# Kernel tuning notes

Measured on AMD Instinct MI355X. Metric: run time of the kernel, lower is better.

## Reference

```python
import jax, jax.numpy as jnp
import numpy as np

D_MODEL = 1024
N_HEADS = 16
N_KV_HEADS = 4
HEAD_DIM = 64


def setup_inputs() -> dict:
    key = jax.random.key(0)
    ks = jax.random.split(key, 5)
    B, T, P = 2, 512, 8
    scale = 1.0 / np.sqrt(D_MODEL)
    return {
        "hidden_states": jax.random.normal(ks[0], (B, T, P, D_MODEL), dtype=jnp.float32),
        # weights stored [in, out] so y = x @ W (same math as nn.Linear with W^T)
        "Wq": jax.random.normal(ks[1], (D_MODEL, N_HEADS * HEAD_DIM), dtype=jnp.float32) * scale,
        "Wk": jax.random.normal(ks[2], (D_MODEL, N_KV_HEADS * HEAD_DIM), dtype=jnp.float32) * scale,
        "Wv": jax.random.normal(ks[3], (D_MODEL, N_KV_HEADS * HEAD_DIM), dtype=jnp.float32) * scale,
        "Wo": jax.random.normal(ks[4], (N_HEADS * HEAD_DIM, D_MODEL), dtype=jnp.float32) * scale,
    }


def _rope_tables(T, d):
    half = d // 2
    inv_freq = 1.0 / (10000.0 ** (jnp.arange(half, dtype=jnp.float32) / half))
    pos = jnp.arange(T, dtype=jnp.float32)
    angles = pos[:, None] * inv_freq[None, :]  # (T, half)
    return jnp.cos(angles), jnp.sin(angles)


def _apply_rope(x, cos, sin):
    # x: (B, P, T, H, d); cos/sin: (T, d/2)
    half = x.shape[-1] // 2
    x1, x2 = x[..., :half], x[..., half:]
    c = cos[None, None, :, None, :]
    s = sin[None, None, :, None, :]
    return jnp.concatenate([x1 * c - x2 * s, x1 * s + x2 * c], axis=-1)


def reference(hidden_states, Wq, Wk, Wv, Wo):
    B, T, P, _ = hidden_states.shape
    x = jnp.transpose(hidden_states, (0, 2, 1, 3))  # (B, P, T, C)
    q = (x @ Wq).reshape(B, P, T, N_HEADS, HEAD_DIM)
    k = (x @ Wk).reshape(B, P, T, N_KV_HEADS, HEAD_DIM)
    v = (x @ Wv).reshape(B, P, T, N_KV_HEADS, HEAD_DIM)

    rep = N_HEADS // N_KV_HEADS
    k = jnp.repeat(k, rep, axis=3)  # (B,P,T,H,d) interleaved like torch repeat/view
    v = jnp.repeat(v, rep, axis=3)

    cos, sin = _rope_tables(T, HEAD_DIM)
    q = _apply_rope(q, cos, sin)
    k = _apply_rope(k, cos, sin)

    # (B,P,H,T,d)
    q = jnp.transpose(q, (0, 1, 3, 2, 4))
    k = jnp.transpose(k, (0, 1, 3, 2, 4))
    v = jnp.transpose(v, (0, 1, 3, 2, 4))

    attn = jnp.einsum("bphqd,bphkd->bphqk", q, k) / jnp.sqrt(
        jnp.asarray(HEAD_DIM, q.dtype))
    attn = jax.nn.softmax(attn, axis=-1)
    out = jnp.einsum("bphqk,bphkd->bphqd", attn, v)
    out = jnp.transpose(out, (0, 1, 3, 2, 4)).reshape(B, P, T, N_HEADS * HEAD_DIM)
    out = jnp.transpose(out, (0, 2, 1, 3))  # (B, T, P, H*d)
    return out @ Wo
```

## Files before the change

kernel.cpp:

```cpp
#include <hip/hip_runtime.h>
#include <stdint.h>


typedef __attribute__((ext_vector_type(8))) short bf16x8;
typedef __attribute__((ext_vector_type(4))) float f32x4;
typedef __attribute__((ext_vector_type(16))) float f32x16;
typedef __attribute__((ext_vector_type(4))) unsigned short us4;
typedef __attribute__((ext_vector_type(8))) unsigned short us8;

static __device__ __forceinline__ unsigned short f2bf(float f) {
  unsigned u = __float_as_uint(f);
  u += 0x7fffu + ((u >> 16) & 1u);
  return (unsigned short)(u >> 16);
}

static __device__ __forceinline__ void ld_lds16(const void* g, void* l) {
  __builtin_amdgcn_global_load_lds(
      (const __attribute__((address_space(1))) void*)g,
      (__attribute__((address_space(3))) void*)l, 16, 0, 0);
}

static __device__ __forceinline__ f32x4 mfma16(bf16x8 a, bf16x8 b, f32x4 c) {
  return __builtin_amdgcn_mfma_f32_16x16x32_bf16(a, b, c, 0, 0, 0);
}
static __device__ __forceinline__ f32x16 mfma32(bf16x8 a, bf16x8 b, f32x16 c) {
  return __builtin_amdgcn_mfma_f32_32x32x16_bf16(a, b, c, 0, 0, 0);
}

__global__ __launch_bounds__(256) void conv_all(
    const float* __restrict__ hs, const float* __restrict__ Wq,
    const float* __restrict__ Wk, const float* __restrict__ Wv,
    const float* __restrict__ Wo, unsigned short* __restrict__ xb,
    unsigned short* __restrict__ wqkv, unsigned short* __restrict__ wot) {
  __shared__ float tile[64][65];
  int bid = blockIdx.x, tid = threadIdx.x;
  if (bid < 8192) {
    int gid = bid * 256 + tid;
    size_t e = (size_t)gid * 4;
    int r = (int)(e >> 10);
    int d = (int)(e & 1023);
    int b = r >> 12, p = (r >> 9) & 7, t = r & 511;
    const float4* src = (const float4*)(hs + ((((size_t)b * 512 + t) * 8 + p) << 10) + d);
    float4 v = *src;
    us4 o;
    o.x = f2bf(v.x); o.y = f2bf(v.y); o.z = f2bf(v.z); o.w = f2bf(v.w);
    *(us4*)(xb + e) = o;
    return;
  }
  int tb = bid - 8192;
  const float* W; unsigned short* Wt; int N, tc0, tn0;
  if (tb < 256)      { W = Wq; Wt = wqkv;                       N = 1024; tc0 = (tb >> 4) * 64;          tn0 = (tb & 15) * 64; }
  else if (tb < 320) { W = Wk; Wt = wqkv + (size_t)1024 * 1024; N = 256;  tc0 = ((tb - 256) >> 2) * 64;  tn0 = ((tb - 256) & 3) * 64; }
  else if (tb < 384) { W = Wv; Wt = wqkv + (size_t)1280 * 1024; N = 256;  tc0 = ((tb - 320) >> 2) * 64;  tn0 = ((tb - 320) & 3) * 64; }
  else               { W = Wo; Wt = wot;                        N = 1024; tc0 = ((tb - 384) >> 4) * 64;  tn0 = ((tb - 384) & 15) * 64; }
  int tr = tid >> 4, tc = tid & 15;
#pragma unroll
  for (int i = 0; i < 4; ++i) {
    int c = tr + i * 16;
    float4 v = *(const float4*)(W + (size_t)(tc0 + c) * N + tn0 + tc * 4);
    tile[c][tc * 4 + 0] = v.x; tile[c][tc * 4 + 1] = v.y;
    tile[c][tc * 4 + 2] = v.z; tile[c][tc * 4 + 3] = v.w;
  }
  __syncthreads();
#pragma unroll
  for (int i = 0; i < 4; ++i) {
    int n = tr + i * 16;
    us4 o;
    o.x = f2bf(tile[tc * 4 + 0][n]); o.y = f2bf(tile[tc * 4 + 1][n]);
    o.z = f2bf(tile[tc * 4 + 2][n]); o.w = f2bf(tile[tc * 4 + 3][n]);
    *(us4*)(Wt + (size_t)(tn0 + n) * 1024 + tc0 + tc * 4) = o;
  }
}

__global__ __launch_bounds__(512, 2) void gemm_qkv(
    const unsigned short* __restrict__ A, const unsigned short* __restrict__ Bt,
    unsigned short* __restrict__ qb, unsigned short* __restrict__ kb,
    unsigned short* __restrict__ vtb) {
  constexpr int K = 1024;
  constexpr int KT = K / 64;
  __shared__ __align__(16) unsigned short Sm[2][2][256 * 64];
  unsigned short* Cs = &Sm[0][0][0];

  int tid = threadIdx.x;
  int lane = tid & 63, wid = tid >> 6;
  int quad = lane >> 4, lo = lane & 15;
  int wg = (blockIdx.x & 7) * 24 + (blockIdx.x >> 3);
  int tn = wg % 6, tm = wg / 6;
  int wr = wid >> 2, wc = wid & 3;
  int srow = lane >> 3, schunk = lane & 7;
  int cg = schunk ^ srow;

  const unsigned short* pa = A + ((size_t)(tm * 256) + wid * 8 + srow) * K + cg * 8;
  const unsigned short* pb = Bt + ((size_t)(tn * 256) + wid * 8 + srow) * K + cg * 8;

  f32x4 z = {0.f, 0.f, 0.f, 0.f};
  f32x4 acc[8][4];
#pragma unroll
  for (int i = 0; i < 8; ++i)
#pragma unroll
    for (int j = 0; j < 4; ++j) acc[i][j] = z;

  auto stage = [&](int t, int p) {
#pragma unroll
    for (int i = 0; i < 4; ++i) {
      ld_lds16(pa + (size_t)i * 64 * K + t * 64,
               (char*)&Sm[p][0][0] + (wid * 8 + i * 64) * 128);
      ld_lds16(pb + (size_t)i * 64 * K + t * 64,
               (char*)&Sm[p][1][0] + (wid * 8 + i * 64) * 128);
    }
  };

  stage(0, 0);
  stage(1, 1);
  asm volatile("s_waitcnt vmcnt(8)" ::: "memory");
  asm volatile("s_barrier" ::: "memory");

  bf16x8 af[4][2], bb0[2][2], bb1[2][2];

  for (int t = 0; t < KT; ++t) {
    int p = t & 1;
    const unsigned short* As = &Sm[p][0][0];
    const unsigned short* Bs = &Sm[p][1][0];

#pragma unroll
    for (int mi = 0; mi < 4; ++mi)
#pragma unroll
      for (int kx = 0; kx < 2; ++kx) {
        int row = wr * 128 + mi * 16 + lo;
        int cgx = (quad + kx * 4) ^ (row & 7);
        af[mi][kx] = *(const bf16x8*)(As + (size_t)row * 64 + cgx * 8);
      }
#pragma unroll
    for (int ni = 0; ni < 2; ++ni)
#pragma unroll
      for (int kx = 0; kx < 2; ++kx) {
        int row = wc * 64 + ni * 16 + lo;
        int cgx = (quad + kx * 4) ^ (row & 7);
        bb0[ni][kx] = *(const bf16x8*)(Bs + (size_t)row * 64 + cgx * 8);
      }
    asm volatile("s_barrier" ::: "memory");
    __builtin_amdgcn_s_setprio(1);
#pragma unroll
    for (int kx = 0; kx < 2; ++kx)
#pragma unroll
      for (int mi = 0; mi < 4; ++mi)
#pragma unroll
        for (int ni = 0; ni < 2; ++ni)
          acc[mi][ni] = mfma16(af[mi][kx], bb0[ni][kx], acc[mi][ni]);
    __builtin_amdgcn_s_setprio(0);
    asm volatile("s_barrier" ::: "memory");

#pragma unroll
    for (int ni = 0; ni < 2; ++ni)
#pragma unroll
      for (int kx = 0; kx < 2; ++kx) {
        int row = wc * 64 + (ni + 2) * 16 + lo;
        int cgx = (quad + kx * 4) ^ (row & 7);
        bb1[ni][kx] = *(const bf16x8*)(Bs + (size_t)row * 64 + cgx * 8);
      }
    asm volatile("s_barrier" ::: "memory");
    __builtin_amdgcn_s_setprio(1);
#pragma unroll
    for (int kx = 0; kx < 2; ++kx)
#pragma unroll
      for (int mi = 0; mi < 4; ++mi)
#pragma unroll
        for (int ni = 0; ni < 2; ++ni)
          acc[mi][ni + 2] = mfma16(af[mi][kx], bb1[ni][kx], acc[mi][ni + 2]);
    __builtin_amdgcn_s_setprio(0);
    asm volatile("s_barrier" ::: "memory");

#pragma unroll
    for (int mi = 0; mi < 4; ++mi)
#pragma unroll
      for (int kx = 0; kx < 2; ++kx) {
        int row = wr * 128 + 64 + mi * 16 + lo;
        int cgx = (quad + kx * 4) ^ (row & 7);
        af[mi][kx] = *(const bf16x8*)(As + (size_t)row * 64 + cgx * 8);
      }
    asm volatile("s_barrier" ::: "memory");
    __builtin_amdgcn_s_setprio(1);
#pragma unroll
    for (int kx = 0; kx < 2; ++kx)
#pragma unroll
      for (int mi = 0; mi < 4; ++mi)
#pragma unroll
        for (int ni = 0; ni < 2; ++ni)
          acc[mi + 4][ni + 2] = mfma16(af[mi][kx], bb1[ni][kx], acc[mi + 4][ni + 2]);
    __builtin_amdgcn_s_setprio(0);
    asm volatile("s_barrier" ::: "memory");

    bool pf = (t + 2 < KT);
    if (pf) stage(t + 2, p);
    __builtin_amdgcn_s_setprio(1);
#pragma unroll
    for (int kx = 0; kx < 2; ++kx)
#pragma unroll
      for (int mi = 0; mi < 4; ++mi)
#pragma unroll
        for (int ni = 0; ni < 2; ++ni)
          acc[mi + 4][ni] = mfma16(af[mi][kx], bb0[ni][kx], acc[mi + 4][ni]);
    __builtin_amdgcn_s_setprio(0);
    if (pf) asm volatile("s_waitcnt vmcnt(8)" ::: "memory");
    else    asm volatile("s_waitcnt vmcnt(0)" ::: "memory");
    asm volatile("s_barrier" ::: "memory");
  }

  if (tn < 5) {
    float qscale = (tn < 4) ? 0.125f : 1.0f;
#pragma unroll
    for (int mi = 0; mi < 8; ++mi)
#pragma unroll
      for (int r = 0; r < 4; ++r) {
        int row = wr * 128 + mi * 16 + quad * 4 + r;
        int tpos = (tm * 256 + row) & 511;
#pragma unroll
        for (int ni = 0; ni < 2; ++ni) {
          float invf = exp2f((float)(ni * 16 + lo) * -0.41524101186092029f);
          float ang = (float)tpos * invf;
          float s, c;
          __sincosf(ang, &s, &c);
          float x1 = acc[mi][ni][r], x2 = acc[mi][ni + 2][r];
          acc[mi][ni][r]     = (x1 * c - x2 * s) * qscale;
          acc[mi][ni + 2][r] = (x1 * s + x2 * c) * qscale;
        }
      }
#pragma unroll
    for (int mi = 0; mi < 8; ++mi)
#pragma unroll
      for (int ni = 0; ni < 4; ++ni)
#pragma unroll
        for (int r = 0; r < 4; ++r) {
          int row = wr * 128 + mi * 16 + quad * 4 + r;
          int col = wc * 64 + ni * 16 + lo;
          int cs = col ^ (((row >> 2) & 3) << 3);
          Cs[row * 256 + cs] = f2bf(acc[mi][ni][r]);
        }
    __syncthreads();
    int tc = tid & 31, ro = tid >> 5;
#pragma unroll
    for (int it = 0; it < 16; ++it) {
      int row = ro + 16 * it;
      int cs = (tc * 8) ^ (((row >> 2) & 3) << 3);
      us8 v = *(const us8*)(Cs + row * 256 + cs);
      size_t grow = (size_t)(tm * 256 + row);
      if (tn < 4) *(us8*)(qb + grow * 1024 + tn * 256 + tc * 8) = v;
      else        *(us8*)(kb + grow * 256 + tc * 8) = v;
    }
  } else {
#pragma unroll
    for (int mi = 0; mi < 8; ++mi)
#pragma unroll
      for (int ni = 0; ni < 4; ++ni)
#pragma unroll
        for (int r = 0; r < 4; ++r) {
          int trow = wr * 128 + mi * 16 + quad * 4 + r;
          int col = wc * 64 + ni * 16 + lo;
          Cs[col * 256 + (trow ^ ((col & 7) << 3))] = f2bf(acc[mi][ni][r]);
        }
    __syncthreads();
    int t0 = (tid & 31) * 8, colIdx = tid >> 5;
    int bp = tm >> 1, tbase = (tm & 1) * 256;
#pragma unroll
    for (int it = 0; it < 16; ++it) {
      int col = colIdx + it * 16;
      us8 v = *(const us8*)(Cs + col * 256 + (t0 ^ ((col & 7) << 3)));
      int hh = col >> 6, dd = col & 63;
      *(us8*)(vtb + (((size_t)(bp * 4 + hh)) * 64 + dd) * 512 + tbase + t0) = v;
    }
  }
}

__global__ __launch_bounds__(512, 2) void gemm_o(
    const unsigned short* __restrict__ A, const unsigned short* __restrict__ Bt,
    float* __restrict__ out) {
  constexpr int K = 1024;
  constexpr int KT = K / 64;
  __shared__ __align__(16) unsigned short Sm[2][(128 + 256) * 64];

  int tid = threadIdx.x;
  int lane = tid & 63, wid = tid >> 6;
  int quad = lane >> 4, lo = lane & 15;
  int wg = (blockIdx.x & 7) * 32 + (blockIdx.x >> 3);
  int tn = wg & 3, tm = wg >> 2;
  int wr = wid >> 2, wc = wid & 3;
  int srow = lane >> 3, schunk = lane & 7;
  int cg = schunk ^ srow;

  const unsigned short* pa = A + ((size_t)(tm * 128) + wid * 8 + srow) * K + cg * 8;
  const unsigned short* pb = Bt + ((size_t)(tn * 256) + wid * 8 + srow) * K + cg * 8;

  f32x4 z = {0.f, 0.f, 0.f, 0.f};
  f32x4 acc[4][4];
#pragma unroll
  for (int i = 0; i < 4; ++i)
#pragma unroll
    for (int j = 0; j < 4; ++j) acc[i][j] = z;

  auto stage = [&](int t, int p) {
    unsigned short* As = &Sm[p][0];
    unsigned short* Bs = &Sm[p][128 * 64];
#pragma unroll
    for (int i = 0; i < 2; ++i)
      ld_lds16(pa + (size_t)i * 64 * K + t * 64,
               (char*)As + (wid * 8 + i * 64) * 128);
#pragma unroll
    for (int i = 0; i < 4; ++i)
      ld_lds16(pb + (size_t)i * 64 * K + t * 64,
               (char*)Bs + (wid * 8 + i * 64) * 128);
  };

  stage(0, 0);
  stage(1, 1);
  asm volatile("s_waitcnt vmcnt(6)" ::: "memory");
  asm volatile("s_barrier" ::: "memory");

  bf16x8 af[4][2], bb0[2][2], bb1[2][2];

  for (int t = 0; t < KT; ++t) {
    int p = t & 1;
    const unsigned short* As = &Sm[p][0];
    const unsigned short* Bs = &Sm[p][128 * 64];

#pragma unroll
    for (int mi = 0; mi < 4; ++mi)
#pragma unroll
      for (int kx = 0; kx < 2; ++kx) {
        int row = wr * 64 + mi * 16 + lo;
        int cgx = (quad + kx * 4) ^ (row & 7);
        af[mi][kx] = *(const bf16x8*)(As + (size_t)row * 64 + cgx * 8);
      }
#pragma unroll
    for (int ni = 0; ni < 2; ++ni)
#pragma unroll
      for (int kx = 0; kx < 2; ++kx) {
        int row = wc * 64 + ni * 16 + lo;
        int cgx = (quad + kx * 4) ^ (row & 7);
        bb0[ni][kx] = *(const bf16x8*)(Bs + (size_t)row * 64 + cgx * 8);
      }
    asm volatile("s_barrier" ::: "memory");
    __builtin_amdgcn_s_setprio(1);
#pragma unroll
    for (int kx = 0; kx < 2; ++kx)
#pragma unroll
      for (int mi = 0; mi < 4; ++mi)
#pragma unroll
        for (int ni = 0; ni < 2; ++ni)
          acc[mi][ni] = mfma16(af[mi][kx], bb0[ni][kx], acc[mi][ni]);
    __builtin_amdgcn_s_setprio(0);
    asm volatile("s_barrier" ::: "memory");

#pragma unroll
    for (int ni = 0; ni < 2; ++ni)
#pragma unroll
      for (int kx = 0; kx < 2; ++kx) {
        int row = wc * 64 + (ni + 2) * 16 + lo;
        int cgx = (quad + kx * 4) ^ (row & 7);
        bb1[ni][kx] = *(const bf16x8*)(Bs + (size_t)row * 64 + cgx * 8);
      }
    asm volatile("s_barrier" ::: "memory");
    __builtin_amdgcn_s_setprio(1);
#pragma unroll
    for (int kx = 0; kx < 2; ++kx)
#pragma unroll
      for (int mi = 0; mi < 4; ++mi)
#pragma unroll
        for (int ni = 0; ni < 2; ++ni)
          acc[mi][ni + 2] = mfma16(af[mi][kx], bb1[ni][kx], acc[mi][ni + 2]);
    __builtin_amdgcn_s_setprio(0);
    asm volatile("s_barrier" ::: "memory");

    bool pf = (t + 2 < KT);
    if (pf) {
      stage(t + 2, p);
      asm volatile("s_waitcnt vmcnt(6)" ::: "memory");
    } else {
      asm volatile("s_waitcnt vmcnt(0)" ::: "memory");
    }
    asm volatile("s_barrier" ::: "memory");
  }

#pragma unroll
  for (int mi = 0; mi < 4; ++mi) {
    for (int ni = 0; ni < 4; ++ni) {
      int col = tn * 256 + wc * 64 + ni * 16 + lo;
      for (int r = 0; r < 4; ++r) {
        int grow = tm * 128 + wr * 64 + mi * 16 + quad * 4 + r;
        int bp = grow >> 9, tt = grow & 511;
        int b = bp >> 3, pp = bp & 7;
        out[((((size_t)b * 512 + tt) * 8 + pp) << 10) + col] = acc[mi][ni][r];
      }
    }
  }
}

__global__ __launch_bounds__(512, 4) void attn(
    const unsigned short* __restrict__ qb, const unsigned short* __restrict__ kb,
    const unsigned short* __restrict__ vtb, unsigned short* __restrict__ ao) {
  __shared__ __align__(16) unsigned short Qs[256 * 64];
  __shared__ __align__(16) unsigned short Ks[2][64 * 64];
  __shared__ __align__(16) unsigned short Vs[2][64 * 64];

  int tid = threadIdx.x;
  int lane = tid & 63, wid = tid >> 6;
  int lo32 = lane & 31, hl = lane >> 5;
  int wg = (blockIdx.x & 7) * 64 + (blockIdx.x >> 3);
  int qt = wg & 1, bph = wg >> 1;
  int head = bph & 15, bp = bph >> 4;
  int kvh = head >> 2;
  int t0 = qt * 256;
  int srow = lane >> 3, schunk = lane & 7;

  const unsigned short* qg = qb + ((size_t)(bp * 512 + t0)) * 1024 + head * 64;
  const unsigned short* kg = kb + ((size_t)bp * 512) * 256 + kvh * 64;
  const unsigned short* vg = vtb + ((size_t)(bp * 4 + kvh)) * 64 * 512;

#pragma unroll
  for (int i = 0; i < 4; ++i) {
    int row = wid * 8 + i * 64 + srow;
    int cg = schunk ^ (row & 7);
    ld_lds16(qg + (size_t)row * 1024 + cg * 8, (char*)Qs + (wid * 8 + i * 64) * 128);
  }

  auto stageKV = [&](int kt, int p) {
    int row = wid * 8 + srow;
    int cg = schunk ^ (row & 7);
    ld_lds16(kg + (size_t)(kt * 64 + row) * 256 + cg * 8, (char*)&Ks[p][0] + (wid * 8) * 128);
    ld_lds16(vg + (size_t)row * 512 + kt * 64 + cg * 8, (char*)&Vs[p][0] + (wid * 8) * 128);
  };

  stageKV(0, 0);
  stageKV(1, 1);
  asm volatile("s_waitcnt vmcnt(2)" ::: "memory");
  asm volatile("s_barrier" ::: "memory");

  f32x16 z16 = {0.f};
  f32x16 o0 = z16, o1 = z16;
  float psum = 0.f;
  int qrow = wid * 32 + lo32;

  for (int kt = 0; kt < 8; ++kt) {
    int p = kt & 1;
    const unsigned short* Kp = &Ks[p][0];
    const unsigned short* Vp = &Vs[p][0];

    f32x16 st0 = z16, st1 = z16;
#pragma unroll
    for (int kkc = 0; kkc < 4; ++kkc) {
      int ch = 2 * kkc + hl;
      bf16x8 qf = *(const bf16x8*)(Qs + (size_t)qrow * 64 + ((ch ^ (qrow & 7)) * 8));
      bf16x8 kf0 = *(const bf16x8*)(Kp + (size_t)lo32 * 64 + ((ch ^ (lo32 & 7)) * 8));
      bf16x8 kf1 = *(const bf16x8*)(Kp + (size_t)(32 + lo32) * 64 + ((ch ^ (lo32 & 7)) * 8));
      st0 = mfma32(kf0, qf, st0);
      st1 = mfma32(kf1, qf, st1);
    }

#pragma unroll
    for (int t = 0; t < 2; ++t) {
      const f32x16& stv = t ? st1 : st0;
      unsigned pk[8], xpk[8];
#pragma unroll
      for (int pp = 0; pp < 8; ++pp) {
        float e0 = __expf(stv[2 * pp]);
        float e1 = __expf(stv[2 * pp + 1]);
        psum += e0 + e1;
        pk[pp] = ((__float_as_uint(e0) + 0x8000u) >> 16) |
                 ((__float_as_uint(e1) + 0x8000u) & 0xffff0000u);
      }
#pragma unroll
      for (int pp = 0; pp < 8; ++pp) xpk[pp] = (unsigned)__shfl_xor((int)pk[pp], 32);
#pragma unroll
      for (int cc = 0; cc < 2; ++cc) {
        int o = cc * 4;
        union { unsigned u[4]; bf16x8 v; } af;
        if (hl == 0) {
          af.u[0] = pk[o];      af.u[1] = pk[o + 1];
          af.u[2] = xpk[o];     af.u[3] = xpk[o + 1];
        } else {
          af.u[0] = xpk[o + 2]; af.u[1] = xpk[o + 3];
          af.u[2] = pk[o + 2];  af.u[3] = pk[o + 3];
        }
        int vch = 2 * (t * 2 + cc) + hl;
        bf16x8 v0 = *(const bf16x8*)(Vp + (size_t)lo32 * 64 + ((vch ^ (lo32 & 7)) * 8));
        bf16x8 v1 = *(const bf16x8*)(Vp + (size_t)(32 + lo32) * 64 + ((vch ^ (lo32 & 7)) * 8));
        o0 = mfma32(af.v, v0, o0);
        o1 = mfma32(af.v, v1, o1);
      }
    }

    if (kt == 7) break;
    asm volatile("s_barrier" ::: "memory");
    if (kt < 6) {
      stageKV(kt + 2, p);
      asm volatile("s_waitcnt vmcnt(2)" ::: "memory");
    } else {
      asm volatile("s_waitcnt vmcnt(0)" ::: "memory");
    }
    asm volatile("s_barrier" ::: "memory");
  }

  psum += __shfl_xor(psum, 32);
  float inv = 1.f / psum;
#pragma unroll
  for (int r = 0; r < 16; ++r) {
    int q_r = (r & 3) + 8 * (r >> 2) + 4 * hl;
    float sc = __shfl(inv, q_r);
    size_t grow = (size_t)(bp * 512 + t0 + wid * 32 + q_r);
    ao[grow * 1024 + head * 64 + lo32]      = f2bf(o0[r] * sc);
    ao[grow * 1024 + head * 64 + 32 + lo32] = f2bf(o1[r] * sc);
  }
}

extern "C" void kernel_launch(void* const* d_in, const int* in_sizes, int n_in,
                              void* d_out, int out_size, void* d_ws, size_t ws_size,
                              hipStream_t stream) {
  const float* hs = (const float*)d_in[0];
  const float* Wq = (const float*)d_in[1];
  const float* Wk = (const float*)d_in[2];
  const float* Wv = (const float*)d_in[3];
  const float* Wo = (const float*)d_in[4];
  float* out = (float*)d_out;

  unsigned short* xb   = (unsigned short*)d_ws;
  unsigned short* wqkv = xb + (size_t)8192 * 1024;
  unsigned short* wot  = wqkv + (size_t)1536 * 1024;
  unsigned short* qbuf = wot + (size_t)1024 * 1024;
  unsigned short* kbuf = qbuf + (size_t)8192 * 1024;
  unsigned short* vtb  = kbuf + (size_t)8192 * 256;
  unsigned short* ao   = xb;

  conv_all<<<8832, 256, 0, stream>>>(hs, Wq, Wk, Wv, Wo, xb, wqkv, wot);
  gemm_qkv<<<192, 512, 0, stream>>>(xb, wqkv, qbuf, kbuf, vtb);
  attn<<<512, 512, 0, stream>>>(qbuf, kbuf, vtb, ao);
  gemm_o<<<256, 512, 0, stream>>>(ao, wot, out);
}
```

Measured before the change: 181.9 us.

## Process full 512-query block per workgroup with Q fragments held in registers

The attention kernel now gives each workgroup all 512 queries of a (batch, position, head) instead of 256, halving the grid, so each K/V tile staged in LDS is reused across twice as many queries. Q is loaded straight from global memory into registers rather than staged through LDS, and each wave handles two 32-row query groups per K/V tile. This is meant to cut repeated K/V global loads and LDS traffic. In exchange, register pressure goes up (launch bounds drop to 2 blocks per SIMD setting) and there are half as many workgroups, which could leave some of the chip's CUs underused.

```diff
diff --git a/kernel.cpp b/kernel.cpp
--- a/kernel.cpp
+++ b/kernel.cpp
@@ -394,39 +394,40 @@
   }
 }
 
-__global__ __launch_bounds__(512, 4) void attn(
-    const unsigned short* __restrict__ qb, const unsigned short* __restrict__ kb,
+__global__ __launch_bounds__(512, 2) void attn(
+    const unsigned short* __restrict__ qbuf, const unsigned short* __restrict__ kb,
     const unsigned short* __restrict__ vtb, unsigned short* __restrict__ ao) {
-  __shared__ __align__(16) unsigned short Qs[256 * 64];
   __shared__ __align__(16) unsigned short Ks[2][64 * 64];
   __shared__ __align__(16) unsigned short Vs[2][64 * 64];
 
   int tid = threadIdx.x;
   int lane = tid & 63, wid = tid >> 6;
   int lo32 = lane & 31, hl = lane >> 5;
-  int wg = (blockIdx.x & 7) * 64 + (blockIdx.x >> 3);
-  int qt = wg & 1, bph = wg >> 1;
-  int head = bph & 15, bp = bph >> 4;
+  int wg = (blockIdx.x & 7) * 32 + (blockIdx.x >> 3);
+  int head = wg & 15, bp = wg >> 4;
   int kvh = head >> 2;
-  int t0 = qt * 256;
   int srow = lane >> 3, schunk = lane & 7;
 
-  const unsigned short* qg = qb + ((size_t)(bp * 512 + t0)) * 1024 + head * 64;
   const unsigned short* kg = kb + ((size_t)bp * 512) * 256 + kvh * 64;
   const unsigned short* vg = vtb + ((size_t)(bp * 4 + kvh)) * 64 * 512;
 
-#pragma unroll
-  for (int i = 0; i < 4; ++i) {
-    int row = wid * 8 + i * 64 + srow;
-    int cg = schunk ^ (row & 7);
-    ld_lds16(qg + (size_t)row * 1024 + cg * 8, (char*)Qs + (wid * 8 + i * 64) * 128);
+  const unsigned short* qgA =
+      qbuf + ((size_t)(bp * 512 + wid * 64 + lo32)) * 1024 + head * 64;
+  bf16x8 qA[4], qB[4];
+#pragma unroll
+  for (int kkc = 0; kkc < 4; ++kkc) {
+    int ch = 2 * kkc + hl;
+    qA[kkc] = *(const bf16x8*)(qgA + ch * 8);
+    qB[kkc] = *(const bf16x8*)(qgA + (size_t)32 * 1024 + ch * 8);
   }
 
   auto stageKV = [&](int kt, int p) {
     int row = wid * 8 + srow;
     int cg = schunk ^ (row & 7);
-    ld_lds16(kg + (size_t)(kt * 64 + row) * 256 + cg * 8, (char*)&Ks[p][0] + (wid * 8) * 128);
-    ld_lds16(vg + (size_t)row * 512 + kt * 64 + cg * 8, (char*)&Vs[p][0] + (wid * 8) * 128);
+    ld_lds16(kg + (size_t)(kt * 64 + row) * 256 + cg * 8,
+             (char*)&Ks[p][0] + (wid * 8) * 128);
+    ld_lds16(vg + (size_t)row * 512 + kt * 64 + cg * 8,
+             (char*)&Vs[p][0] + (wid * 8) * 128);
   };
 
   stageKV(0, 0);
@@ -435,56 +436,71 @@
   asm volatile("s_barrier" ::: "memory");
 
   f32x16 z16 = {0.f};
-  f32x16 o0 = z16, o1 = z16;
-  float psum = 0.f;
-  int qrow = wid * 32 + lo32;
+  f32x16 oA0 = z16, oA1 = z16, oB0 = z16, oB1 = z16;
+  float psumA = 0.f, psumB = 0.f;
 
   for (int kt = 0; kt < 8; ++kt) {
     int p = kt & 1;
     const unsigned short* Kp = &Ks[p][0];
     const unsigned short* Vp = &Vs[p][0];
 
-    f32x16 st0 = z16, st1 = z16;
+    f32x16 sA0 = z16, sA1 = z16, sB0 = z16, sB1 = z16;
 #pragma unroll
     for (int kkc = 0; kkc < 4; ++kkc) {
       int ch = 2 * kkc + hl;
-      bf16x8 qf = *(const bf16x8*)(Qs + (size_t)qrow * 64 + ((ch ^ (qrow & 7)) * 8));
       bf16x8 kf0 = *(const bf16x8*)(Kp + (size_t)lo32 * 64 + ((ch ^ (lo32 & 7)) * 8));
       bf16x8 kf1 = *(const bf16x8*)(Kp + (size_t)(32 + lo32) * 64 + ((ch ^ (lo32 & 7)) * 8));
-      st0 = mfma32(kf0, qf, st0);
-      st1 = mfma32(kf1, qf, st1);
+      sA0 = mfma32(kf0, qA[kkc], sA0);
+      sA1 = mfma32(kf1, qA[kkc], sA1);
+      sB0 = mfma32(kf0, qB[kkc], sB0);
+      sB1 = mfma32(kf1, qB[kkc], sB1);
     }
 
 #pragma unroll
     for (int t = 0; t < 2; ++t) {
-      const f32x16& stv = t ? st1 : st0;
-      unsigned pk[8], xpk[8];
+      const f32x16& svA = t ? sA1 : sA0;
+      const f32x16& svB = t ? sB1 : sB0;
+      unsigned pkA[8], xpA[8], pkB[8], xpB[8];
 #pragma unroll
       for (int pp = 0; pp < 8; ++pp) {
-        float e0 = __expf(stv[2 * pp]);
-        float e1 = __expf(stv[2 * pp + 1]);
-        psum += e0 + e1;
-        pk[pp] = ((__float_as_uint(e0) + 0x8000u) >> 16) |
-                 ((__float_as_uint(e1) + 0x8000u) & 0xffff0000u);
-      }
-#pragma unroll
-      for (int pp = 0; pp < 8; ++pp) xpk[pp] = (unsigned)__shfl_xor((int)pk[pp], 32);
+        float a0 = __expf(svA[2 * pp]);
+        float a1 = __expf(svA[2 * pp + 1]);
+        psumA += a0 + a1;
+        pkA[pp] = ((__float_as_uint(a0) + 0x8000u) >> 16) |
+                  ((__float_as_uint(a1) + 0x8000u) & 0xffff0000u);
+        float b0 = __expf(svB[2 * pp]);
+        float b1 = __expf(svB[2 * pp + 1]);
+        psumB += b0 + b1;
+        pkB[pp] = ((__float_as_uint(b0) + 0x8000u) >> 16) |
+                  ((__float_as_uint(b1) + 0x8000u) & 0xffff0000u);
+      }
+#pragma unroll
+      for (int pp = 0; pp < 8; ++pp) {
+        xpA[pp] = (unsigned)__shfl_xor((int)pkA[pp], 32);
+        xpB[pp] = (unsigned)__shfl_xor((int)pkB[pp], 32);
+      }
 #pragma unroll
       for (int cc = 0; cc < 2; ++cc) {
         int o = cc * 4;
-        union { unsigned u[4]; bf16x8 v; } af;
+        union { unsigned u[4]; bf16x8 v; } fA, fB;
         if (hl == 0) {
-          af.u[0] = pk[o];      af.u[1] = pk[o + 1];
-          af.u[2] = xpk[o];     af.u[3] = xpk[o + 1];
+          fA.u[0] = pkA[o];     fA.u[1] = pkA[o + 1];
+          fA.u[2] = xpA[o];     fA.u[3] = xpA[o + 1];
+          fB.u[0] = pkB[o];     fB.u[1] = pkB[o + 1];
+          fB.u[2] = xpB[o];     fB.u[3] = xpB[o + 1];
         } else {
-          af.u[0] = xpk[o + 2]; af.u[1] = xpk[o + 3];
-          af.u[2] = pk[o + 2];  af.u[3] = pk[o + 3];
+          fA.u[0] = xpA[o + 2]; fA.u[1] = xpA[o + 3];
+          fA.u[2] = pkA[o + 2]; fA.u[3] = pkA[o + 3];
+          fB.u[0] = xpB[o + 2]; fB.u[1] = xpB[o + 3];
+          fB.u[2] = pkB[o + 2]; fB.u[3] = pkB[o + 3];
         }
         int vch = 2 * (t * 2 + cc) + hl;
         bf16x8 v0 = *(const bf16x8*)(Vp + (size_t)lo32 * 64 + ((vch ^ (lo32 & 7)) * 8));
         bf16x8 v1 = *(const bf16x8*)(Vp + (size_t)(32 + lo32) * 64 + ((vch ^ (lo32 & 7)) * 8));
-        o0 = mfma32(af.v, v0, o0);
-        o1 = mfma32(af.v, v1, o1);
+        oA0 = mfma32(fA.v, v0, oA0);
+        oA1 = mfma32(fA.v, v1, oA1);
+        oB0 = mfma32(fB.v, v0, oB0);
+        oB1 = mfma32(fB.v, v1, oB1);
       }
     }
 
@@ -499,15 +515,20 @@
     asm volatile("s_barrier" ::: "memory");
   }
 
-  psum += __shfl_xor(psum, 32);
-  float inv = 1.f / psum;
+  psumA += __shfl_xor(psumA, 32);
+  psumB += __shfl_xor(psumB, 32);
+  float invA = 1.f / psumA, invB = 1.f / psumB;
 #pragma unroll
   for (int r = 0; r < 16; ++r) {
     int q_r = (r & 3) + 8 * (r >> 2) + 4 * hl;
-    float sc = __shfl(inv, q_r);
-    size_t grow = (size_t)(bp * 512 + t0 + wid * 32 + q_r);
-    ao[grow * 1024 + head * 64 + lo32]      = f2bf(o0[r] * sc);
-    ao[grow * 1024 + head * 64 + 32 + lo32] = f2bf(o1[r] * sc);
+    float scA = __shfl(invA, q_r);
+    float scB = __shfl(invB, q_r);
+    size_t gA = (size_t)(bp * 512 + wid * 64 + q_r);
+    ao[gA * 1024 + head * 64 + lo32]      = f2bf(oA0[r] * scA);
+    ao[gA * 1024 + head * 64 + 32 + lo32] = f2bf(oA1[r] * scA);
+    size_t gB = gA + 32;
+    ao[gB * 1024 + head * 64 + lo32]      = f2bf(oB0[r] * scB);
+    ao[gB * 1024 + head * 64 + 32 + lo32] = f2bf(oB1[r] * scB);
   }
 }
 
@@ -531,6 +552,6 @@
 
   conv_all<<<8832, 256, 0, stream>>>(hs, Wq, Wk, Wv, Wo, xb, wqkv, wot);
   gemm_qkv<<<192, 512, 0, stream>>>(xb, wqkv, qbuf, kbuf, vtb);
-  attn<<<512, 512, 0, stream>>>(qbuf, kbuf, vtb, ao);
+  attn<<<256, 512, 0, stream>>>(qbuf, kbuf, vtb, ao);
   gemm_o<<<256, 512, 0, stream>>>(ao, wot, out);
 }
```

After: 179.5 us. About the same (-1.3%).
